# Performance work log

Hardware: AMD Instinct MI355X
Metric: run time of the kernel (lower is better)

## Reference

```python
import jax, jax.numpy as jnp
import numpy as np

N_NODES = 50000
N_EDGES = 320000
D_IN = 256
D_OUT = 256


def setup_inputs() -> dict:
    key = jax.random.key(0)
    k1, k2, k3, k4, k5, k6, k7 = jax.random.split(key, 7)
    s = 1.0 / np.sqrt(D_IN)
    return {
        "node_features": jax.random.normal(k1, (N_NODES, D_IN), dtype=jnp.float32),
        "edge_index": jax.random.randint(k2, (2, N_EDGES), 0, N_NODES, dtype=jnp.int64),
        "w1": jax.random.uniform(k3, (D_OUT, D_IN), jnp.float32, -s, s),
        "w2": jax.random.uniform(k4, (D_OUT, D_IN), jnp.float32, -s, s),
        "w3": jax.random.uniform(k5, (D_OUT, D_IN), jnp.float32, -s, s),
        "b3": jax.random.uniform(k6, (D_OUT,), jnp.float32, -s, s),
    }


def reference(node_features, edge_index, w1, w2, w3, b3):
    # GraphSAGE-style conv: project, gather messages from senders,
    # scatter-sum at receivers, project, combine with self term.
    n = node_features.shape[0]
    proj = node_features @ w3.T + b3                 # [N, D_OUT]
    msgs = proj[edge_index[0]]                       # [E, D_OUT] gather senders
    agg = jax.ops.segment_sum(msgs, edge_index[1], num_segments=n)  # [N, D_OUT]
    out = node_features @ w1.T + agg @ w2.T          # [N, D_OUT]
    return out
```

## Files before the change

### kernel.cpp

```cpp
#include <hip/hip_runtime.h>

#define NN 50000
#define NPAD 50048
#define NE 320000
#define D 256
#define CAP 64

typedef __bf16 bf16x8 __attribute__((ext_vector_type(8)));
typedef float f32x4 __attribute__((ext_vector_type(4)));

__device__ __forceinline__ unsigned short f2bf(float f) {
    unsigned u = __builtin_bit_cast(unsigned, f);
    unsigned r = u + 0x7FFFu + ((u >> 16) & 1u);
    return (unsigned short)(r >> 16);
}
__device__ __forceinline__ float bf2f(unsigned short h) {
    return __builtin_bit_cast(float, (unsigned)h << 16);
}

__global__ __launch_bounds__(256) void prep_weights(
        const float* __restrict__ w1, const float* __restrict__ w2,
        const float* __restrict__ w3, const float* __restrict__ b3,
        unsigned short* __restrict__ WTT, float* __restrict__ bvec) {
    const int j = blockIdx.x;
    const int k = threadIdx.x;
    __shared__ float w2row[D];
    __shared__ float red[D];
    w2row[k] = w2[j * D + k];
    __syncthreads();
    float acc = 0.f;
    #pragma unroll 8
    for (int o = 0; o < D; ++o) acc += w2row[o] * w3[o * D + k];
    WTT[(size_t)j * 512 + k]       = f2bf(w1[j * D + k]);
    WTT[(size_t)j * 512 + D + k]   = f2bf(acc);
    red[k] = w2row[k] * b3[k];
    __syncthreads();
    for (int s = 128; s > 0; s >>= 1) {
        if (k < s) red[k] += red[k + s];
        __syncthreads();
    }
    if (k == 0) bvec[j] = red[0];
}

__global__ __launch_bounds__(256) void convert_x(
        const float* __restrict__ x, unsigned short* __restrict__ xbf,
        int* __restrict__ cnt) {
    const size_t gid = (size_t)blockIdx.x * 256 + threadIdx.x;
    if (gid < NN) cnt[gid] = 0;
    const size_t i = gid * 8;
    if (i >= (size_t)NN * D) return;
    const float4 a = *reinterpret_cast<const float4*>(x + i);
    const float4 b = *reinterpret_cast<const float4*>(x + i + 4);
    ushort4 o0 = {f2bf(a.x), f2bf(a.y), f2bf(a.z), f2bf(a.w)};
    ushort4 o1 = {f2bf(b.x), f2bf(b.y), f2bf(b.z), f2bf(b.w)};
    *reinterpret_cast<ushort4*>(xbf + i)     = o0;
    *reinterpret_cast<ushort4*>(xbf + i + 4) = o1;
}

__global__ __launch_bounds__(256) void fill_csr(
        const int* __restrict__ ei, int* __restrict__ csr, int* __restrict__ cnt) {
    const int e = blockIdx.x * 256 + threadIdx.x;
    if (e >= NE) return;
    const int src = ei[e];
    const int dst = ei[NE + e];
    const int pos = atomicAdd(cnt + dst, 1);
    if (pos < CAP) csr[(size_t)dst * CAP + pos] = src;
}

__global__ __launch_bounds__(256) void agg_gather(
        const unsigned short* __restrict__ xbf, const int* __restrict__ csr,
        const int* __restrict__ cnt, unsigned short* __restrict__ aggbf) {
    const int node = blockIdx.x * 4 + (threadIdx.x >> 6);
    const int lane = threadIdx.x & 63;
    if (node >= NN) return;
    int d = cnt[node]; if (d > CAP) d = CAP;
    const int* __restrict__ row = csr + (size_t)node * CAP;
    float a0 = 0.f, a1 = 0.f, a2 = 0.f, a3 = 0.f;
    int i = 0;
    for (; i + 2 <= d; i += 2) {
        const ushort4 v0 = *reinterpret_cast<const ushort4*>(xbf + (size_t)row[i] * D + lane * 4);
        const ushort4 v1 = *reinterpret_cast<const ushort4*>(xbf + (size_t)row[i + 1] * D + lane * 4);
        a0 += bf2f(v0.x) + bf2f(v1.x); a1 += bf2f(v0.y) + bf2f(v1.y);
        a2 += bf2f(v0.z) + bf2f(v1.z); a3 += bf2f(v0.w) + bf2f(v1.w);
    }
    if (i < d) {
        const ushort4 v = *reinterpret_cast<const ushort4*>(xbf + (size_t)row[i] * D + lane * 4);
        a0 += bf2f(v.x); a1 += bf2f(v.y); a2 += bf2f(v.z); a3 += bf2f(v.w);
    }
    ushort4 o = {f2bf(a0), f2bf(a1), f2bf(a2), f2bf(a3)};
    *reinterpret_cast<ushort4*>(aggbf + (size_t)node * D + lane * 4) = o;
}

__global__ __launch_bounds__(256) void gemm_mfma(
        const unsigned short* __restrict__ xbf, const unsigned short* __restrict__ aggbf,
        const unsigned short* __restrict__ WTT, const float* __restrict__ bvec,
        const int* __restrict__ cnt, float* __restrict__ out) {
    __shared__ __align__(16) unsigned short ldsA[2][128 * 64];
    __shared__ __align__(16) unsigned short ldsB[2][128 * 64];

    const int tid  = threadIdx.x;
    const int w    = tid >> 6;
    const int lane = tid & 63;
    const int wm   = w >> 1, wn = w & 1;
    const int mb   = blockIdx.x >> 1;
    const int nb0  = (blockIdx.x & 1) * 128;
    const int gr0  = mb * 128;

    auto stage = [&](int kt, int b) {
        const unsigned short* __restrict__ srcA = (kt < 4) ? xbf : aggbf;
        const int kcA = (kt & 3) * 64;
        const int kcB = kt * 64;
        #pragma unroll
        for (int p = 0; p < 4; ++p) {
            const int idx = p * 256 + w * 64 + lane;
            const int r = idx >> 3, c = idx & 7;
            const int sw = (c ^ (r & 7)) << 3;
            const unsigned short* gpA = srcA + ((size_t)(gr0 + r) << 8) + kcA + sw;
            unsigned short* lpA = &ldsA[b][(p * 256 + w * 64) << 3];
            __builtin_amdgcn_global_load_lds(
                (const __attribute__((address_space(1))) void*)(const void*)gpA,
                (__attribute__((address_space(3))) void*)(void*)lpA, 16, 0, 0);
            const unsigned short* gpB = WTT + ((size_t)(nb0 + r) << 9) + kcB + sw;
            unsigned short* lpB = &ldsB[b][(p * 256 + w * 64) << 3];
            __builtin_amdgcn_global_load_lds(
                (const __attribute__((address_space(1))) void*)(const void*)gpB,
                (__attribute__((address_space(3))) void*)(void*)lpB, 16, 0, 0);
        }
    };

    f32x4 acc[4][4];
    #pragma unroll
    for (int a = 0; a < 4; ++a)
        #pragma unroll
        for (int b = 0; b < 4; ++b) acc[a][b] = (f32x4)0.f;

    stage(0, 0);
    __syncthreads();
    #pragma unroll 2
    for (int kt = 0; kt < 8; ++kt) {
        const int cur = kt & 1;
        if (kt < 7) stage(kt + 1, cur ^ 1);
        #pragma unroll
        for (int kh = 0; kh < 2; ++kh) {
            const int cbase = kh * 4 + (lane >> 4);
            bf16x8 af[4], bfr[4];
            #pragma unroll
            for (int f = 0; f < 4; ++f) {
                const int ra = wm * 64 + f * 16 + (lane & 15);
                af[f] = *reinterpret_cast<const bf16x8*>(
                    &ldsA[cur][ra * 64 + ((cbase ^ (ra & 7)) << 3)]);
                const int rb = wn * 64 + f * 16 + (lane & 15);
                bfr[f] = *reinterpret_cast<const bf16x8*>(
                    &ldsB[cur][rb * 64 + ((cbase ^ (rb & 7)) << 3)]);
            }
            #pragma unroll
            for (int fm = 0; fm < 4; ++fm)
                #pragma unroll
                for (int fn = 0; fn < 4; ++fn)
                    acc[fm][fn] = __builtin_amdgcn_mfma_f32_16x16x32_bf16(
                        af[fm], bfr[fn], acc[fm][fn], 0, 0, 0);
        }
        __syncthreads();
    }

    const int col0 = nb0 + wn * 64 + (lane & 15);
    float bv[4];
    #pragma unroll
    for (int fn = 0; fn < 4; ++fn) bv[fn] = bvec[col0 + fn * 16];
    #pragma unroll
    for (int fm = 0; fm < 4; ++fm) {
        #pragma unroll
        for (int i = 0; i < 4; ++i) {
            const int row = gr0 + wm * 64 + fm * 16 + ((lane >> 4) << 2) + i;
            if (row < NN) {
                const float dg = (float)cnt[row];
                float* op = out + ((size_t)row << 8) + col0;
                #pragma unroll
                for (int fn = 0; fn < 4; ++fn)
                    op[fn * 16] = acc[fm][fn][i] + dg * bv[fn];
            }
        }
    }
}

extern "C" void kernel_launch(void* const* d_in, const int* in_sizes, int n_in,
                              void* d_out, int out_size, void* d_ws, size_t ws_size,
                              hipStream_t stream) {
    const float* x  = (const float*)d_in[0];
    const int*   ei = (const int*)d_in[1];
    const float* w1 = (const float*)d_in[2];
    const float* w2 = (const float*)d_in[3];
    const float* w3 = (const float*)d_in[4];
    const float* b3 = (const float*)d_in[5];
    float* out = (float*)d_out;

    unsigned short* xbf   = (unsigned short*)d_ws;
    unsigned short* aggbf = xbf + (size_t)NPAD * D;
    unsigned short* WTT   = aggbf + (size_t)NPAD * D;
    float* bvec = (float*)(WTT + (size_t)D * 512);
    int*   cnt  = (int*)(bvec + D);
    int*   csr  = cnt + NN;

    prep_weights<<<D, 256, 0, stream>>>(w1, w2, w3, b3, WTT, bvec);
    convert_x<<<(NN * D) / (256 * 8), 256, 0, stream>>>(x, xbf, cnt);
    fill_csr<<<(NE + 255) / 256, 256, 0, stream>>>(ei, csr, cnt);
    agg_gather<<<(NN + 3) / 4, 256, 0, stream>>>(xbf, csr, cnt, aggbf);
    gemm_mfma<<<((NN + 127) / 128) * 2, 256, 0, stream>>>(xbf, aggbf, WTT, bvec, cnt, out);
}
```

Measured before the change: 112.0 us.

## Fuse convert and CSR build, widen gather loads, drop LDS staging in GEMM

Moves the zeroing of the degree counters into prep_weights and merges the bf16 conversion and CSR fill into one launch split by block index, so one kernel launch disappears. The aggregation kernel now uses 32 lanes per node with 16-byte loads, so each block handles more nodes. The GEMM drops LDS double buffering and reads MFMA fragments straight from global memory into registers, with 64-row blocks covering all 256 output columns. This removes LDS traffic and barriers but relies on cache hits for operand reuse and leaves global load latency exposed.

```diff
diff --git a/kernel.cpp b/kernel.cpp
--- a/kernel.cpp
+++ b/kernel.cpp
@@ -5,6 +5,7 @@
 #define NE 320000
 #define D 256
 #define CAP 64
+#define NCONV 6250
 
 typedef __bf16 bf16x8 __attribute__((ext_vector_type(8)));
 typedef float f32x4 __attribute__((ext_vector_type(4)));
@@ -14,16 +15,25 @@
     unsigned r = u + 0x7FFFu + ((u >> 16) & 1u);
     return (unsigned short)(r >> 16);
 }
-__device__ __forceinline__ float bf2f(unsigned short h) {
-    return __builtin_bit_cast(float, (unsigned)h << 16);
+__device__ __forceinline__ float bflo(unsigned u) {
+    return __builtin_bit_cast(float, u << 16);
+}
+__device__ __forceinline__ float bfhi(unsigned u) {
+    return __builtin_bit_cast(float, u & 0xFFFF0000u);
+}
+__device__ __forceinline__ unsigned packbf(float lo, float hi) {
+    return (unsigned)f2bf(lo) | ((unsigned)f2bf(hi) << 16);
 }
 
 __global__ __launch_bounds__(256) void prep_weights(
         const float* __restrict__ w1, const float* __restrict__ w2,
         const float* __restrict__ w3, const float* __restrict__ b3,
-        unsigned short* __restrict__ WTT, float* __restrict__ bvec) {
+        unsigned short* __restrict__ WTT, float* __restrict__ bvec,
+        int* __restrict__ cnt) {
     const int j = blockIdx.x;
     const int k = threadIdx.x;
+    const int g = j * 256 + k;
+    if (g < NN) cnt[g] = 0;
     __shared__ float w2row[D];
     __shared__ float red[D];
     w2row[k] = w2[j * D + k];
@@ -31,8 +41,8 @@
     float acc = 0.f;
     #pragma unroll 8
     for (int o = 0; o < D; ++o) acc += w2row[o] * w3[o * D + k];
-    WTT[(size_t)j * 512 + k]       = f2bf(w1[j * D + k]);
-    WTT[(size_t)j * 512 + D + k]   = f2bf(acc);
+    WTT[(size_t)j * 512 + k]     = f2bf(w1[j * D + k]);
+    WTT[(size_t)j * 512 + D + k] = f2bf(acc);
     red[k] = w2row[k] * b3[k];
     __syncthreads();
     for (int s = 128; s > 0; s >>= 1) {
@@ -42,91 +52,69 @@
     if (k == 0) bvec[j] = red[0];
 }
 
-__global__ __launch_bounds__(256) void convert_x(
+__global__ __launch_bounds__(256) void convert_and_csr(
         const float* __restrict__ x, unsigned short* __restrict__ xbf,
-        int* __restrict__ cnt) {
-    const size_t gid = (size_t)blockIdx.x * 256 + threadIdx.x;
-    if (gid < NN) cnt[gid] = 0;
-    const size_t i = gid * 8;
-    if (i >= (size_t)NN * D) return;
-    const float4 a = *reinterpret_cast<const float4*>(x + i);
-    const float4 b = *reinterpret_cast<const float4*>(x + i + 4);
-    ushort4 o0 = {f2bf(a.x), f2bf(a.y), f2bf(a.z), f2bf(a.w)};
-    ushort4 o1 = {f2bf(b.x), f2bf(b.y), f2bf(b.z), f2bf(b.w)};
-    *reinterpret_cast<ushort4*>(xbf + i)     = o0;
-    *reinterpret_cast<ushort4*>(xbf + i + 4) = o1;
-}
-
-__global__ __launch_bounds__(256) void fill_csr(
         const int* __restrict__ ei, int* __restrict__ csr, int* __restrict__ cnt) {
-    const int e = blockIdx.x * 256 + threadIdx.x;
-    if (e >= NE) return;
-    const int src = ei[e];
-    const int dst = ei[NE + e];
-    const int pos = atomicAdd(cnt + dst, 1);
-    if (pos < CAP) csr[(size_t)dst * CAP + pos] = src;
+    const int b = blockIdx.x;
+    if (b < NCONV) {
+        const size_t i = ((size_t)b * 256 + threadIdx.x) * 8;
+        const float4 a0 = *reinterpret_cast<const float4*>(x + i);
+        const float4 a1 = *reinterpret_cast<const float4*>(x + i + 4);
+        ushort4 o0 = {f2bf(a0.x), f2bf(a0.y), f2bf(a0.z), f2bf(a0.w)};
+        ushort4 o1 = {f2bf(a1.x), f2bf(a1.y), f2bf(a1.z), f2bf(a1.w)};
+        *reinterpret_cast<ushort4*>(xbf + i)     = o0;
+        *reinterpret_cast<ushort4*>(xbf + i + 4) = o1;
+    } else {
+        const int e = (b - NCONV) * 256 + threadIdx.x;
+        if (e < NE) {
+            const int src = ei[e];
+            const int dst = ei[NE + e];
+            const int pos = atomicAdd(cnt + dst, 1);
+            if (pos < CAP) csr[(size_t)dst * CAP + pos] = src;
+        }
+    }
 }
 
 __global__ __launch_bounds__(256) void agg_gather(
         const unsigned short* __restrict__ xbf, const int* __restrict__ csr,
         const int* __restrict__ cnt, unsigned short* __restrict__ aggbf) {
-    const int node = blockIdx.x * 4 + (threadIdx.x >> 6);
-    const int lane = threadIdx.x & 63;
+    const int node = blockIdx.x * 8 + (threadIdx.x >> 5);
+    const int l32  = threadIdx.x & 31;
     if (node >= NN) return;
     int d = cnt[node]; if (d > CAP) d = CAP;
     const int* __restrict__ row = csr + (size_t)node * CAP;
     float a0 = 0.f, a1 = 0.f, a2 = 0.f, a3 = 0.f;
+    float a4 = 0.f, a5 = 0.f, a6 = 0.f, a7 = 0.f;
     int i = 0;
     for (; i + 2 <= d; i += 2) {
-        const ushort4 v0 = *reinterpret_cast<const ushort4*>(xbf + (size_t)row[i] * D + lane * 4);
-        const ushort4 v1 = *reinterpret_cast<const ushort4*>(xbf + (size_t)row[i + 1] * D + lane * 4);
-        a0 += bf2f(v0.x) + bf2f(v1.x); a1 += bf2f(v0.y) + bf2f(v1.y);
-        a2 += bf2f(v0.z) + bf2f(v1.z); a3 += bf2f(v0.w) + bf2f(v1.w);
+        const uint4 p = *reinterpret_cast<const uint4*>(xbf + (size_t)row[i] * D + l32 * 8);
+        const uint4 q = *reinterpret_cast<const uint4*>(xbf + (size_t)row[i + 1] * D + l32 * 8);
+        a0 += bflo(p.x) + bflo(q.x); a1 += bfhi(p.x) + bfhi(q.x);
+        a2 += bflo(p.y) + bflo(q.y); a3 += bfhi(p.y) + bfhi(q.y);
+        a4 += bflo(p.z) + bflo(q.z); a5 += bfhi(p.z) + bfhi(q.z);
+        a6 += bflo(p.w) + bflo(q.w); a7 += bfhi(p.w) + bfhi(q.w);
     }
     if (i < d) {
-        const ushort4 v = *reinterpret_cast<const ushort4*>(xbf + (size_t)row[i] * D + lane * 4);
-        a0 += bf2f(v.x); a1 += bf2f(v.y); a2 += bf2f(v.z); a3 += bf2f(v.w);
-    }
-    ushort4 o = {f2bf(a0), f2bf(a1), f2bf(a2), f2bf(a3)};
-    *reinterpret_cast<ushort4*>(aggbf + (size_t)node * D + lane * 4) = o;
-}
-
-__global__ __launch_bounds__(256) void gemm_mfma(
+        const uint4 p = *reinterpret_cast<const uint4*>(xbf + (size_t)row[i] * D + l32 * 8);
+        a0 += bflo(p.x); a1 += bfhi(p.x);
+        a2 += bflo(p.y); a3 += bfhi(p.y);
+        a4 += bflo(p.z); a5 += bfhi(p.z);
+        a6 += bflo(p.w); a7 += bfhi(p.w);
+    }
+    uint4 o = {packbf(a0, a1), packbf(a2, a3), packbf(a4, a5), packbf(a6, a7)};
+    *reinterpret_cast<uint4*>(aggbf + (size_t)node * D + l32 * 8) = o;
+}
+
+__global__ __launch_bounds__(256) void gemm_direct(
         const unsigned short* __restrict__ xbf, const unsigned short* __restrict__ aggbf,
         const unsigned short* __restrict__ WTT, const float* __restrict__ bvec,
         const int* __restrict__ cnt, float* __restrict__ out) {
-    __shared__ __align__(16) unsigned short ldsA[2][128 * 64];
-    __shared__ __align__(16) unsigned short ldsB[2][128 * 64];
-
     const int tid  = threadIdx.x;
     const int w    = tid >> 6;
     const int lane = tid & 63;
-    const int wm   = w >> 1, wn = w & 1;
-    const int mb   = blockIdx.x >> 1;
-    const int nb0  = (blockIdx.x & 1) * 128;
-    const int gr0  = mb * 128;
-
-    auto stage = [&](int kt, int b) {
-        const unsigned short* __restrict__ srcA = (kt < 4) ? xbf : aggbf;
-        const int kcA = (kt & 3) * 64;
-        const int kcB = kt * 64;
-        #pragma unroll
-        for (int p = 0; p < 4; ++p) {
-            const int idx = p * 256 + w * 64 + lane;
-            const int r = idx >> 3, c = idx & 7;
-            const int sw = (c ^ (r & 7)) << 3;
-            const unsigned short* gpA = srcA + ((size_t)(gr0 + r) << 8) + kcA + sw;
-            unsigned short* lpA = &ldsA[b][(p * 256 + w * 64) << 3];
-            __builtin_amdgcn_global_load_lds(
-                (const __attribute__((address_space(1))) void*)(const void*)gpA,
-                (__attribute__((address_space(3))) void*)(void*)lpA, 16, 0, 0);
-            const unsigned short* gpB = WTT + ((size_t)(nb0 + r) << 9) + kcB + sw;
-            unsigned short* lpB = &ldsB[b][(p * 256 + w * 64) << 3];
-            __builtin_amdgcn_global_load_lds(
-                (const __attribute__((address_space(1))) void*)(const void*)gpB,
-                (__attribute__((address_space(3))) void*)(void*)lpB, 16, 0, 0);
-        }
-    };
+    const int l16  = lane & 15;
+    const int g4   = lane >> 4;
+    const int gr0  = blockIdx.x * 64;
 
     f32x4 acc[4][4];
     #pragma unroll
@@ -134,36 +122,44 @@
         #pragma unroll
         for (int b = 0; b < 4; ++b) acc[a][b] = (f32x4)0.f;
 
-    stage(0, 0);
-    __syncthreads();
-    #pragma unroll 2
+    #pragma unroll
     for (int kt = 0; kt < 8; ++kt) {
-        const int cur = kt & 1;
-        if (kt < 7) stage(kt + 1, cur ^ 1);
-        #pragma unroll
-        for (int kh = 0; kh < 2; ++kh) {
-            const int cbase = kh * 4 + (lane >> 4);
-            bf16x8 af[4], bfr[4];
+        const int ko = kt * 32 + g4 * 8;
+        bf16x8 af[4], bfr[4];
+        #pragma unroll
+        for (int f = 0; f < 4; ++f) {
+            af[f]  = *reinterpret_cast<const bf16x8*>(
+                xbf + ((size_t)(gr0 + f * 16 + l16) << 8) + ko);
+            bfr[f] = *reinterpret_cast<const bf16x8*>(
+                WTT + ((size_t)(w * 64 + f * 16 + l16) << 9) + ko);
+        }
+        #pragma unroll
+        for (int fm = 0; fm < 4; ++fm)
             #pragma unroll
-            for (int f = 0; f < 4; ++f) {
-                const int ra = wm * 64 + f * 16 + (lane & 15);
-                af[f] = *reinterpret_cast<const bf16x8*>(
-                    &ldsA[cur][ra * 64 + ((cbase ^ (ra & 7)) << 3)]);
-                const int rb = wn * 64 + f * 16 + (lane & 15);
-                bfr[f] = *reinterpret_cast<const bf16x8*>(
-                    &ldsB[cur][rb * 64 + ((cbase ^ (rb & 7)) << 3)]);
-            }
+            for (int fn = 0; fn < 4; ++fn)
+                acc[fm][fn] = __builtin_amdgcn_mfma_f32_16x16x32_bf16(
+                    af[fm], bfr[fn], acc[fm][fn], 0, 0, 0);
+    }
+    #pragma unroll
+    for (int kt = 0; kt < 8; ++kt) {
+        const int ko = kt * 32 + g4 * 8;
+        bf16x8 af[4], bfr[4];
+        #pragma unroll
+        for (int f = 0; f < 4; ++f) {
+            af[f]  = *reinterpret_cast<const bf16x8*>(
+                aggbf + ((size_t)(gr0 + f * 16 + l16) << 8) + ko);
+            bfr[f] = *reinterpret_cast<const bf16x8*>(
+                WTT + ((size_t)(w * 64 + f * 16 + l16) << 9) + 256 + ko);
+        }
+        #pragma unroll
+        for (int fm = 0; fm < 4; ++fm)
             #pragma unroll
-            for (int fm = 0; fm < 4; ++fm)
-                #pragma unroll
-                for (int fn = 0; fn < 4; ++fn)
-                    acc[fm][fn] = __builtin_amdgcn_mfma_f32_16x16x32_bf16(
-                        af[fm], bfr[fn], acc[fm][fn], 0, 0, 0);
-        }
-        __syncthreads();
-    }
-
-    const int col0 = nb0 + wn * 64 + (lane & 15);
+            for (int fn = 0; fn < 4; ++fn)
+                acc[fm][fn] = __builtin_amdgcn_mfma_f32_16x16x32_bf16(
+                    af[fm], bfr[fn], acc[fm][fn], 0, 0, 0);
+    }
+
+    const int col0 = w * 64 + l16;
     float bv[4];
     #pragma unroll
     for (int fn = 0; fn < 4; ++fn) bv[fn] = bvec[col0 + fn * 16];
@@ -171,7 +167,7 @@
     for (int fm = 0; fm < 4; ++fm) {
         #pragma unroll
         for (int i = 0; i < 4; ++i) {
-            const int row = gr0 + wm * 64 + fm * 16 + ((lane >> 4) << 2) + i;
+            const int row = gr0 + fm * 16 + g4 * 4 + i;
             if (row < NN) {
                 const float dg = (float)cnt[row];
                 float* op = out + ((size_t)row << 8) + col0;
@@ -201,9 +197,8 @@
     int*   cnt  = (int*)(bvec + D);
     int*   csr  = cnt + NN;
 
-    prep_weights<<<D, 256, 0, stream>>>(w1, w2, w3, b3, WTT, bvec);
-    convert_x<<<(NN * D) / (256 * 8), 256, 0, stream>>>(x, xbf, cnt);
-    fill_csr<<<(NE + 255) / 256, 256, 0, stream>>>(ei, csr, cnt);
-    agg_gather<<<(NN + 3) / 4, 256, 0, stream>>>(xbf, csr, cnt, aggbf);
-    gemm_mfma<<<((NN + 127) / 128) * 2, 256, 0, stream>>>(xbf, aggbf, WTT, bvec, cnt, out);
-}
+    prep_weights<<<D, 256, 0, stream>>>(w1, w2, w3, b3, WTT, bvec, cnt);
+    convert_and_csr<<<NCONV + (NE + 255) / 256, 256, 0, stream>>>(x, xbf, ei, csr, cnt);
+    agg_gather<<<(NN + 7) / 8, 256, 0, stream>>>(xbf, csr, cnt, aggbf);
+    gemm_direct<<<NPAD / 64, 256, 0, stream>>>(xbf, aggbf, WTT, bvec, cnt, out);
+}
```

After: 142.3 us. 27.1% more time.
